# Performance work log

Measured on AMD Instinct MI355X. Metric: run time of the kernel, lower is better.

The kernel has to match this reference:

```python
import jax, jax.numpy as jnp
import numpy as np

# Static config mirroring the torch module
KS_FULL = 5          # stored kernel size per axis (5,5,5) -> k = 125
KS_RUN = 3           # runtime kernel size -> 27 offsets
INC, OUTC = 64, 64   # max (slimmable) channels
RUN_INC, RUN_OUTC = 48, 48  # runtime channel widths
N = 200000           # active voxels (KITTI-scale)
M = 150000           # padded neighbor pairs per kernel offset
K_RUN = KS_RUN ** 3  # 27


def setup_inputs() -> dict:
    key = jax.random.key(0)
    k1, k2, k3, k4, k5 = jax.random.split(key, 5)
    features = jax.random.normal(k1, (N, RUN_INC), dtype=jnp.float32)
    # init_weight: uniform(-std, std), std = 1/sqrt(inc * k)
    std = 1.0 / np.sqrt(INC * KS_FULL ** 3)
    kernel = jax.random.uniform(k2, (KS_FULL ** 3, INC, OUTC), dtype=jnp.float32,
                                minval=-std, maxval=std)
    in_idx = jax.random.randint(k3, (K_RUN, M), 0, N)
    out_idx = jax.random.randint(k4, (K_RUN, M), 0, N)
    mask = jax.random.randint(k5, (K_RUN, M), 0, 2).astype(bool)
    return {"features": features, "kernel": kernel, "in_idx": in_idx,
            "out_idx": out_idx, "mask": mask}


def _slice_kernel(kernel):
    # view (k, inc, outc) -> (ks2, ks1, ks0, inc, outc), take centered runtime sub-kernel
    k5d = kernel.reshape(KS_FULL, KS_FULL, KS_FULL, INC, OUTC)
    s0 = (KS_FULL - KS_RUN) // 2
    sl = slice(s0, s0 + KS_RUN)
    sub = k5d[sl, sl, sl, :RUN_INC, :RUN_OUTC]   # [3,3,3,rin,rout]
    return sub.reshape(K_RUN, RUN_INC, RUN_OUTC)  # [27,rin,rout]


def reference(features, kernel, in_idx, out_idx, mask):
    # features: [N, rin]; kernel: [125, INC, OUTC]
    # in_idx/out_idx/mask: [K, M] rulebook (padded neighbor maps per kernel offset)
    kk = _slice_kernel(kernel)                                  # [K, rin, rout]
    gathered = jnp.where(mask[..., None], features[in_idx], 0.0)  # [K, M, rin]
    partial = jnp.einsum('kmi,kio->kmo', gathered, kk)           # [K, M, rout]
    out = jnp.zeros((N, RUN_OUTC), features.dtype)
    out = out.at[out_idx.reshape(-1)].add(partial.reshape(-1, RUN_OUTC))
    return out
```

## Files before the change

### kernel.cpp

```cpp
#include <hip/hip_runtime.h>
#include <hip/hip_bf16.h>

#define KS_FULL 5
#define INC 64
#define OUTC 64
#define RUN_INC 48
#define RUN_OUTC 48
#define NPTS 200000
#define MPAIR 150000
#define K_RUN 27
#define NPAIRS (K_RUN * MPAIR)
#define NSCAN (NPTS + 1)
#define SCAN_CHUNK 1024
#define NB1 ((NSCAN + SCAN_CHUNK - 1) / SCAN_CHUNK)

#define OFF_COUNTS   0u
#define OFF_OFFSETS  (1u << 20)
#define OFF_CURSOR   (2u << 20)
#define OFF_BSUMS    (3u << 20)
#define OFF_WBF      ((3u << 20) + 65536u)
#define OFF_FBF      (4u << 20)
#define OFF_SORTED_BIG (24u << 20)
#define OFF_SORTED_MID (4u << 20)
#define WS_BIG  ((size_t)OFF_SORTED_BIG + (size_t)NPAIRS * 4)
#define WS_MID  ((size_t)OFF_SORTED_MID + (size_t)NPAIRS * 4)

#define WBF_U4    (K_RUN * 6 * RUN_OUTC)
#define WBF_BYTES (WBF_U4 * 16)
#define KSPLIT    14
#define WLDS_U4   (KSPLIT * 6 * RUN_OUTC)

#define ROWS_PER_WAVE 25
#define ACC_BLOCKS    500

__device__ __forceinline__ unsigned short bf_rne(float x) {
    unsigned u = __float_as_uint(x);
    u += 0x7FFFu + ((u >> 16) & 1u);
    return (unsigned short)(u >> 16);
}
__device__ __forceinline__ unsigned pack2bf(float lo, float hi) {
    return (unsigned)bf_rne(lo) | ((unsigned)bf_rne(hi) << 16);
}

#if defined(__has_builtin)
#if __has_builtin(__builtin_amdgcn_fdot2_f32_bf16)
#define HAVE_DOT2 1
#endif
#endif

#ifdef HAVE_DOT2
typedef __bf16 bf16x2 __attribute__((ext_vector_type(2)));
__device__ __forceinline__ float dot2bf(unsigned w, unsigned f, float c) {
    return __builtin_amdgcn_fdot2_f32_bf16(__builtin_bit_cast(bf16x2, w),
                                           __builtin_bit_cast(bf16x2, f), c, false);
}
#else
__device__ __forceinline__ float dot2bf(unsigned w, unsigned f, float c) {
    c = fmaf(__uint_as_float(w << 16), __uint_as_float(f << 16), c);
    c = fmaf(__uint_as_float(w & 0xFFFF0000u), __uint_as_float(f & 0xFFFF0000u), c);
    return c;
}
#endif

__global__ __launch_bounds__(256) void prep_wbf(
    const float* __restrict__ kernel, unsigned short* __restrict__ wbf)
{
    int t = blockIdx.x * 256 + threadIdx.x;
    if (t >= K_RUN * RUN_INC * RUN_OUTC) return;
    int k = t / (RUN_INC * RUN_OUTC);
    int r = t - k * (RUN_INC * RUN_OUTC);
    int i = r / RUN_OUTC;
    int o = r - i * RUN_OUTC;
    int a = k / 9, b = (k / 3) % 3, c = k % 3;
    int kf = (a + 1) * (KS_FULL * KS_FULL) + (b + 1) * KS_FULL + (c + 1);
    float v = kernel[(size_t)kf * (INC * OUTC) + i * OUTC + o];
    wbf[(((k * 6 + (i >> 3)) * RUN_OUTC + o) << 3) + (i & 7)] = bf_rne(v);
}

__global__ __launch_bounds__(256) void prep_fbf(
    const float4* __restrict__ f4, uint4* __restrict__ fb4)
{
    int t = blockIdx.x * 256 + threadIdx.x;
    if (t >= (NPTS * RUN_INC) / 8) return;
    float4 a = f4[2 * t], b = f4[2 * t + 1];
    uint4 o;
    o.x = pack2bf(a.x, a.y); o.y = pack2bf(a.z, a.w);
    o.z = pack2bf(b.x, b.y); o.w = pack2bf(b.z, b.w);
    fb4[t] = o;
}

__global__ __launch_bounds__(256) void hist_kernel(
    const int4* __restrict__ out_idx4, const int4* __restrict__ mask4,
    int* __restrict__ counts)
{
    int t = blockIdx.x * 256 + threadIdx.x;
    if (t >= MPAIR / 4) return;
    int base = blockIdx.y * (MPAIR / 4) + t;
    int4 mk = mask4[base];
    int4 oi = out_idx4[base];
    if (mk.x) atomicAdd(&counts[oi.x], 1);
    if (mk.y) atomicAdd(&counts[oi.y], 1);
    if (mk.z) atomicAdd(&counts[oi.z], 1);
    if (mk.w) atomicAdd(&counts[oi.w], 1);
}

__global__ __launch_bounds__(256) void scan1_kernel(
    const int* __restrict__ counts, int* __restrict__ offsets,
    int* __restrict__ bsums)
{
    __shared__ int sh[2][256];
    int b = blockIdx.x, t = threadIdx.x;
    int gbase = b * SCAN_CHUNK + t * 4;
    int v0 = (gbase + 0 < NSCAN) ? counts[gbase + 0] : 0;
    int v1 = (gbase + 1 < NSCAN) ? counts[gbase + 1] : 0;
    int v2 = (gbase + 2 < NSCAN) ? counts[gbase + 2] : 0;
    int v3 = (gbase + 3 < NSCAN) ? counts[gbase + 3] : 0;
    int tsum = v0 + v1 + v2 + v3;
    sh[0][t] = tsum;
    __syncthreads();
    int src = 0;
    for (int d = 1; d < 256; d <<= 1) {
        int dst = src ^ 1;
        sh[dst][t] = sh[src][t] + ((t >= d) ? sh[src][t - d] : 0);
        __syncthreads();
        src = dst;
    }
    int incl = sh[src][t];
    int excl = incl - tsum;
    if (t == 255) bsums[b] = incl;
    int run = excl;
    if (gbase + 0 < NSCAN) { offsets[gbase + 0] = run; } run += v0;
    if (gbase + 1 < NSCAN) { offsets[gbase + 1] = run; } run += v1;
    if (gbase + 2 < NSCAN) { offsets[gbase + 2] = run; } run += v2;
    if (gbase + 3 < NSCAN) { offsets[gbase + 3] = run; }
}

__global__ __launch_bounds__(256) void scan2_kernel(int* __restrict__ bsums)
{
    __shared__ int sh[2][256];
    int t = threadIdx.x;
    int v = (t < NB1) ? bsums[t] : 0;
    sh[0][t] = v;
    __syncthreads();
    int src = 0;
    for (int d = 1; d < 256; d <<= 1) {
        int dst = src ^ 1;
        sh[dst][t] = sh[src][t] + ((t >= d) ? sh[src][t - d] : 0);
        __syncthreads();
        src = dst;
    }
    if (t < NB1) bsums[t] = sh[src][t] - v;
}

__global__ __launch_bounds__(256) void scan3_kernel(
    int* __restrict__ offsets, const int* __restrict__ bsums,
    int* __restrict__ cursor)
{
    int gi = blockIdx.x * 256 + threadIdx.x;
    if (gi < NSCAN) {
        int v = offsets[gi] + bsums[gi >> 10];
        offsets[gi] = v;
        if (gi < NPTS) cursor[gi] = v;
    }
}

__global__ __launch_bounds__(256) void fill_kernel(
    const int4* __restrict__ in_idx4, const int4* __restrict__ out_idx4,
    const int4* __restrict__ mask4, int* __restrict__ cursor,
    int* __restrict__ sorted)
{
    int t = blockIdx.x * 256 + threadIdx.x;
    if (t >= MPAIR / 4) return;
    int k = blockIdx.y;
    int base = k * (MPAIR / 4) + t;
    int4 mk = mask4[base];
    int4 oi = out_idx4[base];
    int4 ii = in_idx4[base];
    int kk = k << 18;
    if (mk.x) { int pos = atomicAdd(&cursor[oi.x], 1); sorted[pos] = ii.x | kk; }
    if (mk.y) { int pos = atomicAdd(&cursor[oi.y], 1); sorted[pos] = ii.y | kk; }
    if (mk.z) { int pos = atomicAdd(&cursor[oi.z], 1); sorted[pos] = ii.z | kk; }
    if (mk.w) { int pos = atomicAdd(&cursor[oi.w], 1); sorted[pos] = ii.w | kk; }
}

#define DOT12(wv, fv)                                              \
    do {                                                           \
        a0 = dot2bf(w0.x, fv.x, a0); a0 = dot2bf(w0.y, fv.y, a0);  \
        a0 = dot2bf(w0.z, fv.z, a0); a0 = dot2bf(w0.w, fv.w, a0);  \
        a1 = dot2bf(w1.x, fv.x, a1); a1 = dot2bf(w1.y, fv.y, a1);  \
        a1 = dot2bf(w1.z, fv.z, a1); a1 = dot2bf(w1.w, fv.w, a1);  \
        a2 = dot2bf(w2.x, fv.x, a2); a2 = dot2bf(w2.y, fv.y, a2);  \
        a2 = dot2bf(w2.z, fv.z, a2); a2 = dot2bf(w2.w, fv.w, a2);  \
    } while (0)

__global__ __launch_bounds__(1024, 8) void accum4_kernel(
    const uint4* __restrict__ fbf4,
    const uint4* __restrict__ wbf4,
    const int* __restrict__ offsets,
    const int* __restrict__ sorted,
    float* __restrict__ out)
{
    __shared__ uint4 Wl4[WLDS_U4];
    for (int i = threadIdx.x; i < WLDS_U4; i += 1024) Wl4[i] = wbf4[i];
    __syncthreads();

    const int lane = threadIdx.x & 63;
    const int slot = lane >> 4;
    const int c    = lane & 15;
    const int wgid = blockIdx.x * 16 + (threadIdx.x >> 6);

    const int row0 = wgid * ROWS_PER_WAVE;
    const int row1 = min(row0 + ROWS_PER_WAVE, NPTS);
    if (row0 >= NPTS) return;

    int start = offsets[row0];
    for (int row = row0; row < row1; ++row) {
        const int end = offsets[row + 1];
        float a0 = 0.f, a1 = 0.f, a2 = 0.f;
        for (int p = start; p < end; p += 4) {
            const int ps = p + slot;
            if (ps < end) {
                const int e  = sorted[ps];
                const int fb = (e & 0x3FFFF) * 6;
                const int kk = e >> 18;
                const int wb = kk * (6 * RUN_OUTC);
                if (kk < KSPLIT) {
                    #pragma unroll
                    for (int ic = 0; ic < 6; ++ic) {
                        const uint4 f  = fbf4[fb + ic];
                        const uint4 w0 = Wl4[wb + ic * RUN_OUTC + c];
                        const uint4 w1 = Wl4[wb + ic * RUN_OUTC + c + 16];
                        const uint4 w2 = Wl4[wb + ic * RUN_OUTC + c + 32];
                        DOT12(w, f);
                    }
                } else {
                    #pragma unroll
                    for (int ic = 0; ic < 6; ++ic) {
                        const uint4 f  = fbf4[fb + ic];
                        const uint4 w0 = wbf4[wb + ic * RUN_OUTC + c];
                        const uint4 w1 = wbf4[wb + ic * RUN_OUTC + c + 16];
                        const uint4 w2 = wbf4[wb + ic * RUN_OUTC + c + 32];
                        DOT12(w, f);
                    }
                }
            }
        }
        a0 += __shfl_xor(a0, 16); a0 += __shfl_xor(a0, 32);
        a1 += __shfl_xor(a1, 16); a1 += __shfl_xor(a1, 32);
        a2 += __shfl_xor(a2, 16); a2 += __shfl_xor(a2, 32);
        if (slot == 0) {
            float* orow = out + (size_t)row * RUN_OUTC;
            orow[c]      = a0;
            orow[c + 16] = a1;
            orow[c + 32] = a2;
        }
        start = end;
    }
}

#define PKMAC(acc, word, fx, fy)                                  \
    do {                                                          \
        acc.x = fmaf(__uint_as_float((word) << 16), (fx), acc.x); \
        acc.y = fmaf(__uint_as_float((word) & 0xFFFF0000u), (fy), acc.y); \
    } while (0)

__global__ __launch_bounds__(1024) void accum_mid_kernel(
    const float* __restrict__ features, const unsigned short* __restrict__ wbf,
    const int* __restrict__ offsets, const int* __restrict__ sorted,
    float* __restrict__ out)
{
    extern __shared__ __align__(16) unsigned short Wlds[];
    {
        const uint4* s4 = (const uint4*)wbf;
        uint4* d4 = (uint4*)Wlds;
        for (int i = threadIdx.x; i < WBF_BYTES / 16; i += 1024) d4[i] = s4[i];
    }
    __syncthreads();

    const int wid  = threadIdx.x >> 6;
    const int lane = threadIdx.x & 63;
    const int o    = (lane < RUN_OUTC) ? lane : (lane - RUN_OUTC);

    for (int row = blockIdx.x * 16 + wid; row < NPTS; row += 256 * 16) {
        int p = offsets[row];
        const int end = offsets[row + 1];
        float2 a0 = make_float2(0.f, 0.f), a1 = a0;
        for (; p < end; ++p) {
            const int e = sorted[p];
            const float4* f0 =
                (const float4*)(features + (size_t)(e & 0x3FFFF) * RUN_INC);
            const unsigned short* w0 = Wlds + (((e >> 18) * 6 * RUN_OUTC + o) << 3);
            #pragma unroll
            for (int ic = 0; ic < 6; ++ic) {
                const float4 A0 = f0[ic * 2], A1 = f0[ic * 2 + 1];
                const uint4 wa = *(const uint4*)(w0 + ic * (RUN_OUTC * 8));
                PKMAC(a0, wa.x, A0.x, A0.y);
                PKMAC(a1, wa.y, A0.z, A0.w);
                PKMAC(a0, wa.z, A1.x, A1.y);
                PKMAC(a1, wa.w, A1.z, A1.w);
            }
        }
        if (lane < RUN_OUTC)
            out[(size_t)row * RUN_OUTC + o] = (a0.x + a0.y) + (a1.x + a1.y);
    }
}

__global__ __launch_bounds__(256) void conv_gather_scatter(
    const float* __restrict__ features, const float* __restrict__ kernel,
    const int* __restrict__ in_idx, const int* __restrict__ out_idx,
    const int* __restrict__ mask, float* __restrict__ out)
{
    __shared__ float W[RUN_INC][RUN_OUTC];
    const int k = blockIdx.y;
    const int a = k / 9, b = (k / 3) % 3, c = k % 3;
    const int kf = ((a + 1) * KS_FULL + (b + 1)) * KS_FULL + (c + 1);
    const float* __restrict__ Wsrc = kernel + (size_t)kf * (INC * OUTC);
    for (int e = threadIdx.x; e < RUN_INC * RUN_OUTC; e += 256) {
        const int i = e / RUN_OUTC;
        const int o = e - i * RUN_OUTC;
        W[i][o] = Wsrc[i * OUTC + o];
    }
    __syncthreads();
    const int m = blockIdx.x * 256 + threadIdx.x;
    if (m >= MPAIR) return;
    const int pair = k * MPAIR + m;
    if (!mask[pair]) return;
    const int in_row = in_idx[pair], out_row = out_idx[pair];
    const float4* __restrict__ frow = (const float4*)(features + (size_t)in_row * RUN_INC);
    float f[RUN_INC];
    #pragma unroll
    for (int i = 0; i < RUN_INC / 4; ++i) {
        const float4 v = frow[i];
        f[4 * i] = v.x; f[4 * i + 1] = v.y; f[4 * i + 2] = v.z; f[4 * i + 3] = v.w;
    }
    float acc[RUN_OUTC];
    #pragma unroll
    for (int o = 0; o < RUN_OUTC; ++o) acc[o] = 0.0f;
    #pragma unroll 4
    for (int i = 0; i < RUN_INC; ++i) {
        const float fi = f[i];
        const float4* __restrict__ w4 = (const float4*)(&W[i][0]);
        #pragma unroll
        for (int o4 = 0; o4 < RUN_OUTC / 4; ++o4) {
            const float4 w = w4[o4];
            acc[4 * o4 + 0] = fmaf(fi, w.x, acc[4 * o4 + 0]);
            acc[4 * o4 + 1] = fmaf(fi, w.y, acc[4 * o4 + 1]);
            acc[4 * o4 + 2] = fmaf(fi, w.z, acc[4 * o4 + 2]);
            acc[4 * o4 + 3] = fmaf(fi, w.w, acc[4 * o4 + 3]);
        }
    }
    float* __restrict__ orow = out + (size_t)out_row * RUN_OUTC;
    #pragma unroll
    for (int o = 0; o < RUN_OUTC; ++o) unsafeAtomicAdd(orow + o, acc[o]);
}

extern "C" void kernel_launch(void* const* d_in, const int* in_sizes, int n_in,
                              void* d_out, int out_size, void* d_ws, size_t ws_size,
                              hipStream_t stream) {
    const float* features = (const float*)d_in[0];
    const float* kernel_w = (const float*)d_in[1];
    const int*   in_idx   = (const int*)d_in[2];
    const int*   out_idx  = (const int*)d_in[3];
    const int*   mask     = (const int*)d_in[4];
    float*       out      = (float*)d_out;

    if (ws_size < WS_MID) {
        hipMemsetAsync(out, 0, (size_t)out_size * sizeof(float), stream);
        dim3 grid((MPAIR + 255) / 256, K_RUN);
        conv_gather_scatter<<<grid, 256, 0, stream>>>(
            features, kernel_w, in_idx, out_idx, mask, out);
        return;
    }

    char* ws = (char*)d_ws;
    int*            counts  = (int*)(ws + OFF_COUNTS);
    int*            offsets = (int*)(ws + OFF_OFFSETS);
    int*            cursor  = (int*)(ws + OFF_CURSOR);
    int*            bsums   = (int*)(ws + OFF_BSUMS);
    unsigned short* wbf     = (unsigned short*)(ws + OFF_WBF);
    const bool big = (ws_size >= WS_BIG);
    int* sorted = (int*)(ws + (big ? OFF_SORTED_BIG : OFF_SORTED_MID));

    hipMemsetAsync(counts, 0, (size_t)NSCAN * sizeof(int), stream);

    prep_wbf<<<(K_RUN * RUN_INC * RUN_OUTC + 255) / 256, 256, 0, stream>>>(
        kernel_w, wbf);

    dim3 pgrid((MPAIR / 4 + 255) / 256, K_RUN);
    hist_kernel<<<pgrid, 256, 0, stream>>>(
        (const int4*)out_idx, (const int4*)mask, counts);

    scan1_kernel<<<NB1, 256, 0, stream>>>(counts, offsets, bsums);
    scan2_kernel<<<1, 256, 0, stream>>>(bsums);
    scan3_kernel<<<(NSCAN + 255) / 256, 256, 0, stream>>>(offsets, bsums, cursor);

    fill_kernel<<<pgrid, 256, 0, stream>>>(
        (const int4*)in_idx, (const int4*)out_idx, (const int4*)mask,
        cursor, sorted);

    if (big) {
        uint4* fbf4 = (uint4*)(ws + OFF_FBF);
        prep_fbf<<<((NPTS * RUN_INC / 8) + 255) / 256, 256, 0, stream>>>(
            (const float4*)features, fbf4);
        accum4_kernel<<<ACC_BLOCKS, 1024, 0, stream>>>(
            fbf4, (const uint4*)wbf, offsets, sorted, out);
    } else {
        accum_mid_kernel<<<256, 1024, WBF_BYTES, stream>>>(
            features, wbf, offsets, sorted, out);
    }
}
```

Before: 700.7 us.

## Bucket pairs by 128-row chunk and kernel offset, accumulate chunk rows in LDS

The rulebook sort now buckets pairs by (output chunk of 128 rows, kernel offset) instead of per output row. Each block owns one chunk and splits that chunk's pairs evenly across its 8 waves. Each wave reloads the weight slice into registers only when the offset changes and double-buffers the feature loads. Results are summed with LDS float atomics into a per-chunk tile, then written out coalesced. This removes per-row load imbalance and the repeated LDS/global weight fetches, at the cost of LDS atomic contention, and it drops the mid-size workspace path.

```diff
diff --git a/kernel.cpp b/kernel.cpp
--- a/kernel.cpp
+++ b/kernel.cpp
@@ -10,28 +10,22 @@
 #define MPAIR 150000
 #define K_RUN 27
 #define NPAIRS (K_RUN * MPAIR)
-#define NSCAN (NPTS + 1)
+
+#define CHUNK_ROWS 128
+#define NCHUNK ((NPTS + CHUNK_ROWS - 1) / CHUNK_ROWS)
+#define NBUCK (NCHUNK * K_RUN)
+#define NSCANB (NBUCK + 1)
 #define SCAN_CHUNK 1024
-#define NB1 ((NSCAN + SCAN_CHUNK - 1) / SCAN_CHUNK)
-
-#define OFF_COUNTS   0u
-#define OFF_OFFSETS  (1u << 20)
-#define OFF_CURSOR   (2u << 20)
-#define OFF_BSUMS    (3u << 20)
-#define OFF_WBF      ((3u << 20) + 65536u)
-#define OFF_FBF      (4u << 20)
-#define OFF_SORTED_BIG (24u << 20)
-#define OFF_SORTED_MID (4u << 20)
-#define WS_BIG  ((size_t)OFF_SORTED_BIG + (size_t)NPAIRS * 4)
-#define WS_MID  ((size_t)OFF_SORTED_MID + (size_t)NPAIRS * 4)
-
-#define WBF_U4    (K_RUN * 6 * RUN_OUTC)
-#define WBF_BYTES (WBF_U4 * 16)
-#define KSPLIT    14
-#define WLDS_U4   (KSPLIT * 6 * RUN_OUTC)
-
-#define ROWS_PER_WAVE 25
-#define ACC_BLOCKS    500
+#define NB1 ((NSCANB + SCAN_CHUNK - 1) / SCAN_CHUNK)
+
+#define OFF_COUNTS  0u
+#define OFF_OFFSETS (256u << 10)
+#define OFF_CURSOR  (512u << 10)
+#define OFF_BSUMS   (768u << 10)
+#define OFF_WBF     (832u << 10)
+#define OFF_FBF     (1u << 20)
+#define OFF_SORTED  (21u << 20)
+#define WS_NEED ((size_t)OFF_SORTED + (size_t)NPAIRS * 4)
 
 __device__ __forceinline__ unsigned short bf_rne(float x) {
     unsigned u = __float_as_uint(x);
@@ -95,13 +89,14 @@
 {
     int t = blockIdx.x * 256 + threadIdx.x;
     if (t >= MPAIR / 4) return;
-    int base = blockIdx.y * (MPAIR / 4) + t;
+    int k = blockIdx.y;
+    int base = k * (MPAIR / 4) + t;
     int4 mk = mask4[base];
     int4 oi = out_idx4[base];
-    if (mk.x) atomicAdd(&counts[oi.x], 1);
-    if (mk.y) atomicAdd(&counts[oi.y], 1);
-    if (mk.z) atomicAdd(&counts[oi.z], 1);
-    if (mk.w) atomicAdd(&counts[oi.w], 1);
+    if (mk.x) atomicAdd(&counts[(oi.x >> 7) * K_RUN + k], 1);
+    if (mk.y) atomicAdd(&counts[(oi.y >> 7) * K_RUN + k], 1);
+    if (mk.z) atomicAdd(&counts[(oi.z >> 7) * K_RUN + k], 1);
+    if (mk.w) atomicAdd(&counts[(oi.w >> 7) * K_RUN + k], 1);
 }
 
 __global__ __launch_bounds__(256) void scan1_kernel(
@@ -111,10 +106,10 @@
     __shared__ int sh[2][256];
     int b = blockIdx.x, t = threadIdx.x;
     int gbase = b * SCAN_CHUNK + t * 4;
-    int v0 = (gbase + 0 < NSCAN) ? counts[gbase + 0] : 0;
-    int v1 = (gbase + 1 < NSCAN) ? counts[gbase + 1] : 0;
-    int v2 = (gbase + 2 < NSCAN) ? counts[gbase + 2] : 0;
-    int v3 = (gbase + 3 < NSCAN) ? counts[gbase + 3] : 0;
+    int v0 = (gbase + 0 < NSCANB) ? counts[gbase + 0] : 0;
+    int v1 = (gbase + 1 < NSCANB) ? counts[gbase + 1] : 0;
+    int v2 = (gbase + 2 < NSCANB) ? counts[gbase + 2] : 0;
+    int v3 = (gbase + 3 < NSCANB) ? counts[gbase + 3] : 0;
     int tsum = v0 + v1 + v2 + v3;
     sh[0][t] = tsum;
     __syncthreads();
@@ -129,10 +124,10 @@
     int excl = incl - tsum;
     if (t == 255) bsums[b] = incl;
     int run = excl;
-    if (gbase + 0 < NSCAN) { offsets[gbase + 0] = run; } run += v0;
-    if (gbase + 1 < NSCAN) { offsets[gbase + 1] = run; } run += v1;
-    if (gbase + 2 < NSCAN) { offsets[gbase + 2] = run; } run += v2;
-    if (gbase + 3 < NSCAN) { offsets[gbase + 3] = run; }
+    if (gbase + 0 < NSCANB) { offsets[gbase + 0] = run; } run += v0;
+    if (gbase + 1 < NSCANB) { offsets[gbase + 1] = run; } run += v1;
+    if (gbase + 2 < NSCANB) { offsets[gbase + 2] = run; } run += v2;
+    if (gbase + 3 < NSCANB) { offsets[gbase + 3] = run; }
 }
 
 __global__ __launch_bounds__(256) void scan2_kernel(int* __restrict__ bsums)
@@ -157,10 +152,10 @@
     int* __restrict__ cursor)
 {
     int gi = blockIdx.x * 256 + threadIdx.x;
-    if (gi < NSCAN) {
+    if (gi < NSCANB) {
         int v = offsets[gi] + bsums[gi >> 10];
         offsets[gi] = v;
-        if (gi < NPTS) cursor[gi] = v;
+        if (gi < NBUCK) cursor[gi] = v;
     }
 }
 
@@ -176,132 +171,93 @@
     int4 mk = mask4[base];
     int4 oi = out_idx4[base];
     int4 ii = in_idx4[base];
-    int kk = k << 18;
-    if (mk.x) { int pos = atomicAdd(&cursor[oi.x], 1); sorted[pos] = ii.x | kk; }
-    if (mk.y) { int pos = atomicAdd(&cursor[oi.y], 1); sorted[pos] = ii.y | kk; }
-    if (mk.z) { int pos = atomicAdd(&cursor[oi.z], 1); sorted[pos] = ii.z | kk; }
-    if (mk.w) { int pos = atomicAdd(&cursor[oi.w], 1); sorted[pos] = ii.w | kk; }
-}
-
-#define DOT12(wv, fv)                                              \
-    do {                                                           \
-        a0 = dot2bf(w0.x, fv.x, a0); a0 = dot2bf(w0.y, fv.y, a0);  \
-        a0 = dot2bf(w0.z, fv.z, a0); a0 = dot2bf(w0.w, fv.w, a0);  \
-        a1 = dot2bf(w1.x, fv.x, a1); a1 = dot2bf(w1.y, fv.y, a1);  \
-        a1 = dot2bf(w1.z, fv.z, a1); a1 = dot2bf(w1.w, fv.w, a1);  \
-        a2 = dot2bf(w2.x, fv.x, a2); a2 = dot2bf(w2.y, fv.y, a2);  \
-        a2 = dot2bf(w2.z, fv.z, a2); a2 = dot2bf(w2.w, fv.w, a2);  \
-    } while (0)
-
-__global__ __launch_bounds__(1024, 8) void accum4_kernel(
+    int kk = k << 25;
+    if (mk.x) { int pos = atomicAdd(&cursor[(oi.x >> 7) * K_RUN + k], 1);
+                sorted[pos] = ii.x | ((oi.x & 127) << 18) | kk; }
+    if (mk.y) { int pos = atomicAdd(&cursor[(oi.y >> 7) * K_RUN + k], 1);
+                sorted[pos] = ii.y | ((oi.y & 127) << 18) | kk; }
+    if (mk.z) { int pos = atomicAdd(&cursor[(oi.z >> 7) * K_RUN + k], 1);
+                sorted[pos] = ii.z | ((oi.z & 127) << 18) | kk; }
+    if (mk.w) { int pos = atomicAdd(&cursor[(oi.w >> 7) * K_RUN + k], 1);
+                sorted[pos] = ii.w | ((oi.w & 127) << 18) | kk; }
+}
+
+#define LOADF(Fr, e) do { const uint4* fp_ = fbf4 + (size_t)((e) & 0x3FFFF) * 6; \
+    Fr##0 = fp_[0]; Fr##1 = fp_[1]; Fr##2 = fp_[2];                              \
+    Fr##3 = fp_[3]; Fr##4 = fp_[4]; Fr##5 = fp_[5]; } while (0)
+
+#define LOADW(kk) do { const uint4* wp_ = wbf4 + (size_t)(kk) * (6 * RUN_OUTC) + wo; \
+    w0 = wp_[0]; w1 = wp_[RUN_OUTC]; w2 = wp_[2 * RUN_OUTC];                         \
+    w3 = wp_[3 * RUN_OUTC]; w4 = wp_[4 * RUN_OUTC]; w5 = wp_[5 * RUN_OUTC]; } while (0)
+
+#define DOTIC(Wv, Fv)                                         \
+    a0 = dot2bf(Wv.x, Fv.x, a0); a1 = dot2bf(Wv.y, Fv.y, a1); \
+    a2 = dot2bf(Wv.z, Fv.z, a2); a3 = dot2bf(Wv.w, Fv.w, a3);
+
+#define COMPUTE(Fr, e) do {                                   \
+    float a0 = 0.f, a1 = 0.f, a2 = 0.f, a3 = 0.f;             \
+    DOTIC(w0, Fr##0) DOTIC(w1, Fr##1) DOTIC(w2, Fr##2)        \
+    DOTIC(w3, Fr##3) DOTIC(w4, Fr##4) DOTIC(w5, Fr##5)        \
+    float s_ = (a0 + a1) + (a2 + a3);                         \
+    int rl_ = ((e) >> 18) & (CHUNK_ROWS - 1);                 \
+    if (lane < RUN_OUTC)                                      \
+        atomicAdd(&accS[rl_ * RUN_OUTC + lane], s_);          \
+} while (0)
+
+__global__ __launch_bounds__(512, 4) void accum5_kernel(
     const uint4* __restrict__ fbf4,
     const uint4* __restrict__ wbf4,
     const int* __restrict__ offsets,
     const int* __restrict__ sorted,
-    float* __restrict__ out)
-{
-    __shared__ uint4 Wl4[WLDS_U4];
-    for (int i = threadIdx.x; i < WLDS_U4; i += 1024) Wl4[i] = wbf4[i];
+    float4* __restrict__ out4)
+{
+    __shared__ float accS[CHUNK_ROWS * RUN_OUTC];
+    const int chunk = blockIdx.x;
+    for (int i = threadIdx.x; i < CHUNK_ROWS * RUN_OUTC; i += 512) accS[i] = 0.f;
     __syncthreads();
 
     const int lane = threadIdx.x & 63;
-    const int slot = lane >> 4;
-    const int c    = lane & 15;
-    const int wgid = blockIdx.x * 16 + (threadIdx.x >> 6);
-
-    const int row0 = wgid * ROWS_PER_WAVE;
-    const int row1 = min(row0 + ROWS_PER_WAVE, NPTS);
-    if (row0 >= NPTS) return;
-
-    int start = offsets[row0];
-    for (int row = row0; row < row1; ++row) {
-        const int end = offsets[row + 1];
-        float a0 = 0.f, a1 = 0.f, a2 = 0.f;
-        for (int p = start; p < end; p += 4) {
-            const int ps = p + slot;
-            if (ps < end) {
-                const int e  = sorted[ps];
-                const int fb = (e & 0x3FFFF) * 6;
-                const int kk = e >> 18;
-                const int wb = kk * (6 * RUN_OUTC);
-                if (kk < KSPLIT) {
-                    #pragma unroll
-                    for (int ic = 0; ic < 6; ++ic) {
-                        const uint4 f  = fbf4[fb + ic];
-                        const uint4 w0 = Wl4[wb + ic * RUN_OUTC + c];
-                        const uint4 w1 = Wl4[wb + ic * RUN_OUTC + c + 16];
-                        const uint4 w2 = Wl4[wb + ic * RUN_OUTC + c + 32];
-                        DOT12(w, f);
-                    }
-                } else {
-                    #pragma unroll
-                    for (int ic = 0; ic < 6; ++ic) {
-                        const uint4 f  = fbf4[fb + ic];
-                        const uint4 w0 = wbf4[wb + ic * RUN_OUTC + c];
-                        const uint4 w1 = wbf4[wb + ic * RUN_OUTC + c + 16];
-                        const uint4 w2 = wbf4[wb + ic * RUN_OUTC + c + 32];
-                        DOT12(w, f);
-                    }
-                }
-            }
+    const int wv   = threadIdx.x >> 6;
+    const int wo   = (lane < RUN_OUTC) ? lane : lane - RUN_OUTC;
+    const int S = offsets[chunk * K_RUN];
+    const int E = offsets[(chunk + 1) * K_RUN];
+    const int P = E - S;
+    int p        = S + (int)(((long long)P * wv) >> 3);
+    const int p1 = S + (int)(((long long)P * (wv + 1)) >> 3);
+
+    if (p < p1) {
+        uint4 w0, w1, w2, w3, w4, w5;
+        uint4 fa0, fa1, fa2, fa3, fa4, fa5;
+        uint4 fb0, fb1, fb2, fb3, fb4, fb5;
+        int ec = sorted[p];
+        LOADF(fa, ec);
+        int curk = -1;
+        for (;;) {
+            int pn = (p + 1 < p1) ? p + 1 : p;
+            int en = sorted[pn];
+            LOADF(fb, en);
+            int kk = ec >> 25;
+            if (kk != curk) { curk = kk; LOADW(kk); }
+            COMPUTE(fa, ec);
+            if (++p >= p1) break;
+            int pn2 = (p + 1 < p1) ? p + 1 : p;
+            int en2 = sorted[pn2];
+            LOADF(fa, en2);
+            kk = en >> 25;
+            if (kk != curk) { curk = kk; LOADW(kk); }
+            COMPUTE(fb, en);
+            ec = en2;
+            if (++p >= p1) break;
         }
-        a0 += __shfl_xor(a0, 16); a0 += __shfl_xor(a0, 32);
-        a1 += __shfl_xor(a1, 16); a1 += __shfl_xor(a1, 32);
-        a2 += __shfl_xor(a2, 16); a2 += __shfl_xor(a2, 32);
-        if (slot == 0) {
-            float* orow = out + (size_t)row * RUN_OUTC;
-            orow[c]      = a0;
-            orow[c + 16] = a1;
-            orow[c + 32] = a2;
-        }
-        start = end;
-    }
-}
-
-#define PKMAC(acc, word, fx, fy)                                  \
-    do {                                                          \
-        acc.x = fmaf(__uint_as_float((word) << 16), (fx), acc.x); \
-        acc.y = fmaf(__uint_as_float((word) & 0xFFFF0000u), (fy), acc.y); \
-    } while (0)
-
-__global__ __launch_bounds__(1024) void accum_mid_kernel(
-    const float* __restrict__ features, const unsigned short* __restrict__ wbf,
-    const int* __restrict__ offsets, const int* __restrict__ sorted,
-    float* __restrict__ out)
-{
-    extern __shared__ __align__(16) unsigned short Wlds[];
-    {
-        const uint4* s4 = (const uint4*)wbf;
-        uint4* d4 = (uint4*)Wlds;
-        for (int i = threadIdx.x; i < WBF_BYTES / 16; i += 1024) d4[i] = s4[i];
-    }
-    __syncthreads();
-
-    const int wid  = threadIdx.x >> 6;
-    const int lane = threadIdx.x & 63;
-    const int o    = (lane < RUN_OUTC) ? lane : (lane - RUN_OUTC);
-
-    for (int row = blockIdx.x * 16 + wid; row < NPTS; row += 256 * 16) {
-        int p = offsets[row];
-        const int end = offsets[row + 1];
-        float2 a0 = make_float2(0.f, 0.f), a1 = a0;
-        for (; p < end; ++p) {
-            const int e = sorted[p];
-            const float4* f0 =
-                (const float4*)(features + (size_t)(e & 0x3FFFF) * RUN_INC);
-            const unsigned short* w0 = Wlds + (((e >> 18) * 6 * RUN_OUTC + o) << 3);
-            #pragma unroll
-            for (int ic = 0; ic < 6; ++ic) {
-                const float4 A0 = f0[ic * 2], A1 = f0[ic * 2 + 1];
-                const uint4 wa = *(const uint4*)(w0 + ic * (RUN_OUTC * 8));
-                PKMAC(a0, wa.x, A0.x, A0.y);
-                PKMAC(a1, wa.y, A0.z, A0.w);
-                PKMAC(a0, wa.z, A1.x, A1.y);
-                PKMAC(a1, wa.w, A1.z, A1.w);
-            }
-        }
-        if (lane < RUN_OUTC)
-            out[(size_t)row * RUN_OUTC + o] = (a0.x + a0.y) + (a1.x + a1.y);
+    }
+    __syncthreads();
+
+    const float4* a4 = (const float4*)accS;
+    const int n4 = CHUNK_ROWS * RUN_OUTC / 4;
+    const int base4 = chunk * n4;
+    for (int i = threadIdx.x; i < n4; i += 512) {
+        int g = base4 + i;
+        if (g < NPTS * RUN_OUTC / 4) out4[g] = a4[i];
     }
 }
 
@@ -364,7 +320,7 @@
     const int*   mask     = (const int*)d_in[4];
     float*       out      = (float*)d_out;
 
-    if (ws_size < WS_MID) {
+    if (ws_size < WS_NEED) {
         hipMemsetAsync(out, 0, (size_t)out_size * sizeof(float), stream);
         dim3 grid((MPAIR + 255) / 256, K_RUN);
         conv_gather_scatter<<<grid, 256, 0, stream>>>(
@@ -378,13 +334,15 @@
     int*            cursor  = (int*)(ws + OFF_CURSOR);
     int*            bsums   = (int*)(ws + OFF_BSUMS);
     unsigned short* wbf     = (unsigned short*)(ws + OFF_WBF);
-    const bool big = (ws_size >= WS_BIG);
-    int* sorted = (int*)(ws + (big ? OFF_SORTED_BIG : OFF_SORTED_MID));
-
-    hipMemsetAsync(counts, 0, (size_t)NSCAN * sizeof(int), stream);
+    uint4*          fbf4    = (uint4*)(ws + OFF_FBF);
+    int*            sorted  = (int*)(ws + OFF_SORTED);
+
+    hipMemsetAsync(counts, 0, (size_t)NSCANB * sizeof(int), stream);
 
     prep_wbf<<<(K_RUN * RUN_INC * RUN_OUTC + 255) / 256, 256, 0, stream>>>(
         kernel_w, wbf);
+    prep_fbf<<<((NPTS * RUN_INC / 8) + 255) / 256, 256, 0, stream>>>(
+        (const float4*)features, fbf4);
 
     dim3 pgrid((MPAIR / 4 + 255) / 256, K_RUN);
     hist_kernel<<<pgrid, 256, 0, stream>>>(
@@ -392,20 +350,12 @@
 
     scan1_kernel<<<NB1, 256, 0, stream>>>(counts, offsets, bsums);
     scan2_kernel<<<1, 256, 0, stream>>>(bsums);
-    scan3_kernel<<<(NSCAN + 255) / 256, 256, 0, stream>>>(offsets, bsums, cursor);
+    scan3_kernel<<<(NSCANB + 255) / 256, 256, 0, stream>>>(offsets, bsums, cursor);
 
     fill_kernel<<<pgrid, 256, 0, stream>>>(
         (const int4*)in_idx, (const int4*)out_idx, (const int4*)mask,
         cursor, sorted);
 
-    if (big) {
-        uint4* fbf4 = (uint4*)(ws + OFF_FBF);
-        prep_fbf<<<((NPTS * RUN_INC / 8) + 255) / 256, 256, 0, stream>>>(
-            (const float4*)features, fbf4);
-        accum4_kernel<<<ACC_BLOCKS, 1024, 0, stream>>>(
-            fbf4, (const uint4*)wbf, offsets, sorted, out);
-    } else {
-        accum_mid_kernel<<<256, 1024, WBF_BYTES, stream>>>(
-            features, wbf, offsets, sorted, out);
-    }
-}
+    accum5_kernel<<<NCHUNK, 512, 0, stream>>>(
+        fbf4, (const uint4*)wbf, offsets, sorted, (float4*)out);
+}
```

After: 930.1 us. 32.7% more time.
